# Performance work log

Measured on AMD Instinct MI355X. Metric: run time of the kernel, lower is better.

The kernel has to match this reference:

```python
import jax, jax.numpy as jnp
import numpy as np

N, E = 10000, 160000
IN_C, HID, K = 128, 256, 16


def setup_inputs() -> dict:
    key = jax.random.key(0)
    ks = jax.random.split(key, 8)
    x = jax.random.normal(ks[0], (N, IN_C), jnp.float32)
    edge_index = jax.random.randint(ks[1], (2, E), 0, N, dtype=jnp.int32).astype(jnp.int64)
    edge_attributes = jax.random.uniform(ks[2], (E,), jnp.float32)
    W1 = jax.random.normal(ks[3], (IN_C, HID), jnp.float32) / np.sqrt(IN_C)
    b1 = jnp.zeros((HID,), jnp.float32)
    W2 = jax.random.normal(ks[4], (HID, HID), jnp.float32) / np.sqrt(HID)
    b2 = jnp.zeros((HID,), jnp.float32)
    Wp = jax.random.normal(ks[5], (HID, K), jnp.float32) / np.sqrt(HID)
    bp = jnp.zeros((K,), jnp.float32)
    return dict(x=x, edge_index=edge_index, edge_attributes=edge_attributes,
                W1=W1, b1=b1, W2=W2, b2=b2, Wp=Wp, bp=bp)


def _gcn_conv(x, src, dst, ew, W, b):
    """GCNConv with add_self_loops=True, normalize=True, edge weights."""
    n = x.shape[0]
    loop = jnp.arange(n)
    s = jnp.concatenate([src, loop])
    d = jnp.concatenate([dst, loop])
    w = jnp.concatenate([ew, jnp.ones((n,), x.dtype)])
    deg = jax.ops.segment_sum(w, d, num_segments=n)           # weighted in-degree
    dis = jnp.where(deg > 0, jax.lax.rsqrt(deg), 0.0)         # D^{-1/2}, inf -> 0
    norm = dis[s] * w * dis[d]                                # per-edge coefficient
    h = x @ W                                                 # transform first
    msg = norm[:, None] * h[s]                                # gather from source
    out = jax.ops.segment_sum(msg, d, num_segments=n)         # scatter-add to target
    return out + b


def reference(x, edge_index, edge_attributes, W1, b1, W2, b2, Wp, bp):
    src, dst = edge_index[0], edge_index[1]
    ew = edge_attributes
    h = jax.nn.relu(_gcn_conv(x, src, dst, ew, W1, b1))
    h = jax.nn.relu(_gcn_conv(h, src, dst, ew, W2, b2))

    # to_dense_adj (duplicate edges accumulate)
    adj = jnp.zeros((N, N), h.dtype).at[src, dst].add(ew)

    # DMoNPooling (dropout=0, eval): s = softmax(Linear(h))
    s = jax.nn.softmax(h @ Wp + bp, axis=-1)                  # [N, K]

    out_adj = s.T @ adj @ s                                   # [K, K]
    deg = adj.sum(axis=1)                                     # [N]
    m = deg.sum() / 2
    ca = s.T @ deg[:, None]                                   # [K, 1]
    cb = deg[None, :] @ s                                     # [1, K]
    normalizer = (ca @ cb) / (2 * m)
    spectral_loss = -jnp.trace(out_adj - normalizer) / (2 * m)

    cluster_size = s.sum(axis=0)                              # [K]
    cluster_loss = jnp.linalg.norm(cluster_size) / N * jnp.sqrt(jnp.float32(K)) - 1.0

    loss = 100.0 * (spectral_loss + cluster_loss)
    # PyG returns s with a leading batch dim of 1
    return s[None], loss, 100.0 * spectral_loss, 100.0 * cluster_loss
```

## Files before the change

### kernel.cpp

```cpp
#include <hip/hip_runtime.h>
#include <math.h>


#define ER_BLOCKS 512

typedef unsigned short u16;
typedef __attribute__((ext_vector_type(8))) short short8v;
typedef __attribute__((ext_vector_type(4))) float float4v;
typedef __attribute__((ext_vector_type(4))) unsigned short ushort4v;
typedef __attribute__((ext_vector_type(8))) unsigned short ushort8v;

__device__ __forceinline__ u16 f2bf_rne(float x) {
  unsigned u = __float_as_uint(x);
  u = (u + 0x7fffu + ((u >> 16) & 1u)) >> 16;
  return (u16)u;
}
__device__ __forceinline__ float bf2f(u16 h) {
  return __uint_as_float(((unsigned)h) << 16);
}

__device__ __forceinline__ bool ei_is_i64(const int* __restrict__ ei) {
  return ((ei[1] | ei[3] | ei[5] | ei[7]) == 0);
}
__device__ __forceinline__ int ld_idx(const int* __restrict__ ei, int pos, bool i64) {
  return i64 ? ei[2 * pos] : ei[pos];
}

__global__ __launch_bounds__(256) void setup_kernel(int4* __restrict__ zp, int zn4,
                                                    const float* __restrict__ x,
                                                    u16* __restrict__ xbf, int nx4,
                                                    const float* __restrict__ W1,
                                                    u16* __restrict__ w1hi, u16* __restrict__ w1lo,
                                                    const float* __restrict__ W2,
                                                    u16* __restrict__ w2hi, u16* __restrict__ w2lo) {
  const int T1 = 256 * 128, T2 = 256 * 256;
  int idx = blockIdx.x * 256 + threadIdx.x;
  if (idx < zn4) {
    zp[idx] = make_int4(0, 0, 0, 0);
    return;
  }
  idx -= zn4;
  if (idx < nx4) {
    float4 v = reinterpret_cast<const float4*>(x)[idx];
    ushort4v o = {f2bf_rne(v.x), f2bf_rne(v.y), f2bf_rne(v.z), f2bf_rne(v.w)};
    reinterpret_cast<ushort4v*>(xbf)[idx] = o;
    return;
  }
  idx -= nx4;
  if (idx < T1) {
    int n = idx >> 7, k = idx & 127;
    float v = W1[k * 256 + n];
    u16 h = f2bf_rne(v);
    w1hi[idx] = h;
    w1lo[idx] = f2bf_rne(v - bf2f(h));
    return;
  }
  idx -= T1;
  if (idx < T2) {
    int n = idx >> 8, k = idx & 255;
    float v = W2[k * 256 + n];
    u16 h = f2bf_rne(v);
    w2hi[idx] = h;
    w2lo[idx] = f2bf_rne(v - bf2f(h));
  }
}

__global__ __launch_bounds__(256) void edge_count(const int* __restrict__ ei,
                                                  const float* __restrict__ ew,
                                                  int* __restrict__ cnt,
                                                  float* __restrict__ deg,
                                                  float* __restrict__ wdeg, int E) {
  int e = blockIdx.x * 256 + threadIdx.x;
  if (e >= E) return;
  bool i64 = ei_is_i64(ei);
  int s = ld_idx(ei, e, i64);
  int d = ld_idx(ei, E + e, i64);
  float we = ew[e];
  atomicAdd(&cnt[d], 1);
  atomicAdd(&deg[d], we);
  atomicAdd(&wdeg[s], we);
}

__global__ __launch_bounds__(1024) void scan_kernel(const int* __restrict__ cnt,
                                                    int* __restrict__ rowptr, int n) {
  __shared__ int sums[1024];
  int tid = threadIdx.x;
  int CH = (n + 1023) >> 10;
  int beg = tid * CH, end = min(beg + CH, n);
  int s = 0;
  for (int i = beg; i < end; ++i) s += cnt[i];
  sums[tid] = s;
  __syncthreads();
  for (int off = 1; off < 1024; off <<= 1) {
    int v = (tid >= off) ? sums[tid - off] : 0;
    __syncthreads();
    sums[tid] += v;
    __syncthreads();
  }
  int run = (tid == 0) ? 0 : sums[tid - 1];
  for (int i = beg; i < end; ++i) { rowptr[i] = run; run += cnt[i]; }
  if (tid == 1023) rowptr[n] = run;
}

__global__ __launch_bounds__(256) void scatter_edges(const int* __restrict__ ei,
                                                     const float* __restrict__ ew,
                                                     const int* __restrict__ rowptr,
                                                     int* __restrict__ cur,
                                                     const float* __restrict__ deg,
                                                     int* __restrict__ col,
                                                     float* __restrict__ coef, int E) {
  int e = blockIdx.x * 256 + threadIdx.x;
  if (e >= E) return;
  bool i64 = ei_is_i64(ei);
  int s = ld_idx(ei, e, i64);
  int d = ld_idx(ei, E + e, i64);
  int p = rowptr[d] + atomicAdd(&cur[d], 1);
  col[p] = s;
  float ds = 1.0f / sqrtf(deg[s] + 1.0f);
  float dd = 1.0f / sqrtf(deg[d] + 1.0f);
  coef[p] = ds * ew[e] * dd;
}

template <int CH>
__global__ __launch_bounds__(256) void aggregate_pre(const u16* __restrict__ src,
                                                     const int* __restrict__ rowptr,
                                                     const int* __restrict__ col,
                                                     const float* __restrict__ coef,
                                                     const float* __restrict__ deg,
                                                     u16* __restrict__ ohi,
                                                     u16* __restrict__ olo, int N) {
  constexpr int Q = CH / 8;
  constexpr int NS = 256 / Q;
  int i = blockIdx.x;
  int t = threadIdx.x;
  int q = t % Q, slot = t / Q;
  int e0 = rowptr[i], e1 = rowptr[i + 1];
  float a[8] = {};
  for (int p = e0 + slot; p < e1; p += NS) {
    int c = col[p];
    float w = coef[p];
    ushort8v v = *reinterpret_cast<const ushort8v*>(&src[(size_t)c * CH + q * 8]);
#pragma unroll
    for (int j = 0; j < 8; ++j) a[j] += w * bf2f(v[j]);
  }
  __shared__ float red[256][9];
#pragma unroll
  for (int j = 0; j < 8; ++j) red[t][j] = a[j];
  __syncthreads();
  if (slot == 0) {
#pragma unroll
    for (int s2 = 1; s2 < NS; ++s2)
#pragma unroll
      for (int j = 0; j < 8; ++j) a[j] += red[s2 * Q + q][j];
    float w0 = 1.0f / (deg[i] + 1.0f);
    ushort8v xv = *reinterpret_cast<const ushort8v*>(&src[(size_t)i * CH + q * 8]);
    ushort8v hv, lv;
#pragma unroll
    for (int j = 0; j < 8; ++j) {
      a[j] += w0 * bf2f(xv[j]);
      u16 h = f2bf_rne(a[j]);
      hv[j] = h;
      lv[j] = f2bf_rne(a[j] - bf2f(h));
    }
    *reinterpret_cast<ushort8v*>(&ohi[(size_t)i * CH + q * 8]) = hv;
    *reinterpret_cast<ushort8v*>(&olo[(size_t)i * CH + q * 8]) = lv;
  }
}

__global__ __launch_bounds__(256) void gemm_mfma(const u16* __restrict__ Ahi,
                                                 const u16* __restrict__ Alo,
                                                 const u16* __restrict__ Wthi,
                                                 const u16* __restrict__ Wtlo,
                                                 const float* __restrict__ bias,
                                                 float* __restrict__ C,
                                                 u16* __restrict__ Cbf,
                                                 int M, int K, int outbf) {
  __shared__ u16 As_hi[64][40], As_lo[64][40];
  __shared__ u16 Bs_hi[64][40], Bs_lo[64][40];
  int tid = threadIdx.x;
  int w = tid >> 6, l = tid & 63;
  int wm = w >> 1, wn = w & 1;
  int row0 = blockIdx.x * 64, col0 = blockIdx.y * 64;
  int srow = tid >> 2, sc = (tid & 3) * 8;
  int fr = l & 15, kg = (l >> 4) * 8;

  float4v acc[2][2];
#pragma unroll
  for (int i = 0; i < 2; ++i)
#pragma unroll
    for (int j = 0; j < 2; ++j) acc[i][j] = (float4v){0.f, 0.f, 0.f, 0.f};

  for (int k0 = 0; k0 < K; k0 += 32) {
    {
      int gr = row0 + srow;
      uint4 zero = make_uint4(0, 0, 0, 0);
      uint4 vh = zero, vl = zero;
      if (gr < M) {
        vh = *reinterpret_cast<const uint4*>(&Ahi[(size_t)gr * K + k0 + sc]);
        vl = *reinterpret_cast<const uint4*>(&Alo[(size_t)gr * K + k0 + sc]);
      }
      *reinterpret_cast<uint4*>(&As_hi[srow][sc]) = vh;
      *reinterpret_cast<uint4*>(&As_lo[srow][sc]) = vl;
      int bn = col0 + srow;
      uint4 bh = *reinterpret_cast<const uint4*>(&Wthi[(size_t)bn * K + k0 + sc]);
      uint4 bl = *reinterpret_cast<const uint4*>(&Wtlo[(size_t)bn * K + k0 + sc]);
      *reinterpret_cast<uint4*>(&Bs_hi[srow][sc]) = bh;
      *reinterpret_cast<uint4*>(&Bs_lo[srow][sc]) = bl;
    }
    __syncthreads();
    short8v ah[2], al[2], bh[2], bl[2];
#pragma unroll
    for (int i = 0; i < 2; ++i) {
      int r = wm * 32 + i * 16 + fr;
      ah[i] = *reinterpret_cast<const short8v*>(&As_hi[r][kg]);
      al[i] = *reinterpret_cast<const short8v*>(&As_lo[r][kg]);
    }
#pragma unroll
    for (int j = 0; j < 2; ++j) {
      int n = wn * 32 + j * 16 + fr;
      bh[j] = *reinterpret_cast<const short8v*>(&Bs_hi[n][kg]);
      bl[j] = *reinterpret_cast<const short8v*>(&Bs_lo[n][kg]);
    }
#pragma unroll
    for (int i = 0; i < 2; ++i)
#pragma unroll
      for (int j = 0; j < 2; ++j) {
        acc[i][j] = __builtin_amdgcn_mfma_f32_16x16x32_bf16(ah[i], bh[j], acc[i][j], 0, 0, 0);
        acc[i][j] = __builtin_amdgcn_mfma_f32_16x16x32_bf16(al[i], bh[j], acc[i][j], 0, 0, 0);
        acc[i][j] = __builtin_amdgcn_mfma_f32_16x16x32_bf16(ah[i], bl[j], acc[i][j], 0, 0, 0);
      }
    __syncthreads();
  }
#pragma unroll
  for (int j = 0; j < 2; ++j) {
    int gc = col0 + wn * 32 + j * 16 + fr;
    float bj = bias[gc];
#pragma unroll
    for (int i = 0; i < 2; ++i) {
#pragma unroll
      for (int r = 0; r < 4; ++r) {
        int gr = row0 + wm * 32 + i * 16 + (l >> 4) * 4 + r;
        if (gr < M) {
          float v = fmaxf(acc[i][j][r] + bj, 0.0f);
          if (outbf) Cbf[(size_t)gr * 256 + gc] = f2bf_rne(v);
          else       C[(size_t)gr * 256 + gc] = v;
        }
      }
    }
  }
}

__global__ __launch_bounds__(256) void pool_kernel(const float* __restrict__ h,
                                                   const float* __restrict__ Wp,
                                                   const float* __restrict__ bp,
                                                   const float* __restrict__ wdeg,
                                                   float* __restrict__ s_out,
                                                   float* __restrict__ pp, int N) {
  __shared__ float Wps[256 * 16];
  __shared__ float loc[33];
  int tid = threadIdx.x;
  for (int idx = tid; idx < 4096; idx += 256) Wps[idx] = Wp[idx];
  if (tid < 33) loc[tid] = 0.f;
  __syncthreads();
  int lane = tid & 63;
  int wave = tid >> 6;
  int k = lane & 15, g = lane >> 4;
  int node = blockIdx.x * 16 + wave * 4 + g;
  float acc = 0.f, wd = 0.f;
  if (node < N) {
    wd = wdeg[node];
    const float4* hrow = reinterpret_cast<const float4*>(h + (size_t)node * 256);
#pragma unroll 8
    for (int c4 = 0; c4 < 64; ++c4) {
      float4 hv = hrow[c4];
      int cb = c4 * 4;
      acc += hv.x * Wps[(cb + 0) * 16 + k];
      acc += hv.y * Wps[(cb + 1) * 16 + k];
      acc += hv.z * Wps[(cb + 2) * 16 + k];
      acc += hv.w * Wps[(cb + 3) * 16 + k];
    }
    acc += bp[k];
  }
  float mx = acc;
#pragma unroll
  for (int off = 1; off < 16; off <<= 1) mx = fmaxf(mx, __shfl_xor(mx, off));
  float ex = (node < N) ? expf(acc - mx) : 0.f;
  float sm = ex;
#pragma unroll
  for (int off = 1; off < 16; off <<= 1) sm += __shfl_xor(sm, off);
  float sval = (node < N) ? ex / sm : 0.f;
  if (node < N) s_out[(size_t)node * 16 + k] = sval;
  float v = sval;
  float v2 = wd * sval;
  float v3 = (k == 0) ? wd : 0.f;
  v += __shfl_xor(v, 16);  v += __shfl_xor(v, 32);
  v2 += __shfl_xor(v2, 16); v2 += __shfl_xor(v2, 32);
  v3 += __shfl_xor(v3, 16); v3 += __shfl_xor(v3, 32);
  if (lane < 16) {
    atomicAdd(&loc[lane], v);
    atomicAdd(&loc[16 + lane], v2);
  }
  if (lane == 0) atomicAdd(&loc[32], v3);
  __syncthreads();
  if (tid < 33) pp[(size_t)blockIdx.x * 33 + tid] = loc[tid];
}

__global__ __launch_bounds__(256) void edge_reduce(const int* __restrict__ ei,
                                                   const float* __restrict__ ew,
                                                   const float* __restrict__ s,
                                                   float* __restrict__ part, int E) {
  int tid = threadIdx.x;
  bool i64 = ei_is_i64(ei);
  int le = tid >> 2, sub = tid & 3;
  int epi = gridDim.x * 64;
  float acc = 0.f;
  for (int e = blockIdx.x * 64 + le; e < E; e += epi) {
    int a = ld_idx(ei, e, i64);
    int b = ld_idx(ei, E + e, i64);
    float w = ew[e];
    float4 av = *reinterpret_cast<const float4*>(s + (size_t)a * 16 + sub * 4);
    float4 bv = *reinterpret_cast<const float4*>(s + (size_t)b * 16 + sub * 4);
    float d = av.x * bv.x + av.y * bv.y + av.z * bv.z + av.w * bv.w;
    d += __shfl_xor(d, 1);
    d += __shfl_xor(d, 2);
    acc += w * d;
  }
#pragma unroll
  for (int off = 4; off < 64; off <<= 1) acc += __shfl_xor(acc, off);
  __shared__ float loc;
  if (tid == 0) loc = 0.f;
  __syncthreads();
  if ((tid & 63) == 0) atomicAdd(&loc, acc);
  __syncthreads();
  if (tid == 0) part[blockIdx.x] = loc;
}

__global__ __launch_bounds__(256) void finalize(const float* __restrict__ epart,
                                                const float* __restrict__ pp, int pb,
                                                float* __restrict__ out,
                                                int N, int s_elems) {
  __shared__ float cred[256];
  __shared__ float vals[32];
  __shared__ float scal[2];
  int tid = threadIdx.x;
  float a = 0.f;
  for (int b = tid; b < ER_BLOCKS; b += 256) a += epart[b];
  float wv = 0.f;
  for (int b = tid; b < pb; b += 256) wv += pp[(size_t)b * 33 + 32];
#pragma unroll
  for (int off = 1; off < 64; off <<= 1) {
    a += __shfl_xor(a, off);
    wv += __shfl_xor(wv, off);
  }
  if (tid == 0) { scal[0] = 0.f; scal[1] = 0.f; }
  __syncthreads();
  if ((tid & 63) == 0) {
    atomicAdd(&scal[0], a);
    atomicAdd(&scal[1], wv);
  }
  {
    int k = tid & 31, sl = tid >> 5;
    float c = 0.f;
    for (int b = sl; b < pb; b += 8) c += pp[(size_t)b * 33 + k];
    cred[tid] = c;
  }
  __syncthreads();
  if (tid < 32) {
    float c = cred[tid];
#pragma unroll
    for (int sl = 1; sl < 8; ++sl) c += cred[sl * 32 + tid];
    vals[tid] = c;
  }
  __syncthreads();
  if (tid == 0) {
    float tr = scal[0], m2 = scal[1];
    float ca2 = 0.f, cs2 = 0.f;
    for (int k = 0; k < 16; ++k) {
      cs2 += vals[k] * vals[k];
      ca2 += vals[16 + k] * vals[16 + k];
    }
    float sp = -(tr - ca2 / m2) / m2;
    float cl = sqrtf(cs2) / (float)N * 4.0f - 1.0f;
    out[s_elems + 0] = 100.f * (sp + cl);
    out[s_elems + 1] = 100.f * sp;
    out[s_elems + 2] = 100.f * cl;
  }
}

extern "C" void kernel_launch(void* const* d_in, const int* in_sizes, int n_in,
                              void* d_out, int out_size, void* d_ws, size_t ws_size,
                              hipStream_t stream) {
  const float* x  = (const float*)d_in[0];
  const int*   ei = (const int*)d_in[1];
  const float* ew = (const float*)d_in[2];
  const float* W1 = (const float*)d_in[3];
  const float* b1 = (const float*)d_in[4];
  const float* W2 = (const float*)d_in[5];
  const float* b2 = (const float*)d_in[6];
  const float* Wp = (const float*)d_in[7];
  const float* bp = (const float*)d_in[8];
  float* out = (float*)d_out;

  const int IN_C = 128, HID = 256;
  const int N = in_sizes[0] / IN_C;
  const int E = in_sizes[2];
  const int pool_blocks = (N + 15) / 16;

  char* p = (char*)d_ws;
  auto alloc = [&](size_t b) { char* r = p; p += (b + 255) & ~(size_t)255; return r; };
  float* deg     = (float*)alloc((size_t)N * 4);
  float* wdeg    = (float*)alloc((size_t)N * 4);
  int*   cnt     = (int*)alloc((size_t)N * 4);
  int*   cur     = (int*)alloc((size_t)N * 4);
  char*  zero_end = p;
  u16*   xbf     = (u16*)alloc((size_t)N * IN_C * 2);
  u16*   hbf     = (u16*)alloc((size_t)N * HID * 2);
  u16*   axhi    = (u16*)alloc((size_t)N * IN_C * 2);
  u16*   axlo    = (u16*)alloc((size_t)N * IN_C * 2);
  u16*   ahhi    = (u16*)alloc((size_t)N * HID * 2);
  u16*   ahlo    = (u16*)alloc((size_t)N * HID * 2);
  float* h2      = (float*)alloc((size_t)N * HID * 4);
  u16*   w1hi    = (u16*)alloc((size_t)256 * 128 * 2);
  u16*   w1lo    = (u16*)alloc((size_t)256 * 128 * 2);
  u16*   w2hi    = (u16*)alloc((size_t)256 * 256 * 2);
  u16*   w2lo    = (u16*)alloc((size_t)256 * 256 * 2);
  int*   rowptr  = (int*)alloc((size_t)(N + 1) * 4);
  int*   col     = (int*)alloc((size_t)E * 4);
  float* coef    = (float*)alloc((size_t)E * 4);
  float* epart   = (float*)alloc((size_t)ER_BLOCKS * 4);
  float* pp      = (float*)alloc((size_t)pool_blocks * 33 * 4);
  if ((size_t)(p - (char*)d_ws) > ws_size) return;

  int zn4 = (int)((zero_end - (char*)deg) >> 4);
  int nx4 = (N * IN_C) / 4;
  int setup_items = zn4 + nx4 + 256 * 128 + 256 * 256;
  setup_kernel<<<(setup_items + 255) / 256, 256, 0, stream>>>(
      (int4*)deg, zn4, x, xbf, nx4, W1, w1hi, w1lo, W2, w2hi, w2lo);

  int eb = (E + 255) / 256;
  edge_count<<<eb, 256, 0, stream>>>(ei, ew, cnt, deg, wdeg, E);
  scan_kernel<<<1, 1024, 0, stream>>>(cnt, rowptr, N);
  scatter_edges<<<eb, 256, 0, stream>>>(ei, ew, rowptr, cur, deg, col, coef, E);

  dim3 gg((N + 63) / 64, HID / 64);
  aggregate_pre<128><<<N, 256, 0, stream>>>(xbf, rowptr, col, coef, deg, axhi, axlo, N);
  gemm_mfma<<<gg, 256, 0, stream>>>(axhi, axlo, w1hi, w1lo, b1, nullptr, hbf, N, IN_C, 1);
  aggregate_pre<256><<<N, 256, 0, stream>>>(hbf, rowptr, col, coef, deg, ahhi, ahlo, N);
  gemm_mfma<<<gg, 256, 0, stream>>>(ahhi, ahlo, w2hi, w2lo, b2, h2, nullptr, N, HID, 0);

  pool_kernel<<<pool_blocks, 256, 0, stream>>>(h2, Wp, bp, wdeg, out, pp, N);
  edge_reduce<<<ER_BLOCKS, 256, 0, stream>>>(ei, ew, out, epart, E);
  finalize<<<1, 256, 0, stream>>>(epart, pp, pool_blocks, out, N, N * 16);
}
```

Before: 144.4 us.

## Fuse setup kernels, use wave-per-node aggregation, last-block finalize

Several independent changes. Edge counting is merged with the bf16 conversion kernel and records a per-edge rank, so scatter no longer needs a second atomic counter. The degree rsqrt is computed once per node inside the scan kernel. Aggregation now assigns one wavefront per node and reduces with shuffles instead of a 256-thread block with shared-memory reduction. The finalize kernel is folded into edge_reduce via a last-block atomic counter. These aim to cut launch count, atomics, shared-memory syncs and idle threads on low-degree nodes, at the cost of an extra rank buffer and a threadfence-based completion pattern.

Measured after the change: 178.8 us. 1.24x slower.

```diff
diff --git a/kernel.cpp b/kernel.cpp
--- a/kernel.cpp
+++ b/kernel.cpp
@@ -26,20 +26,39 @@
   return i64 ? ei[2 * pos] : ei[pos];
 }
 
-__global__ __launch_bounds__(256) void setup_kernel(int4* __restrict__ zp, int zn4,
-                                                    const float* __restrict__ x,
-                                                    u16* __restrict__ xbf, int nx4,
-                                                    const float* __restrict__ W1,
-                                                    u16* __restrict__ w1hi, u16* __restrict__ w1lo,
-                                                    const float* __restrict__ W2,
-                                                    u16* __restrict__ w2hi, u16* __restrict__ w2lo) {
+__global__ __launch_bounds__(256) void zero_init(int4* __restrict__ p, int n4) {
+  int i = blockIdx.x * 256 + threadIdx.x;
+  if (i < n4) p[i] = make_int4(0, 0, 0, 0);
+}
+
+__global__ __launch_bounds__(256) void count_convert(const int* __restrict__ ei,
+                                                     const float* __restrict__ ew,
+                                                     int* __restrict__ cnt,
+                                                     float* __restrict__ deg,
+                                                     float* __restrict__ wdeg,
+                                                     int* __restrict__ rank, int E,
+                                                     const float* __restrict__ x,
+                                                     u16* __restrict__ xbf, int nx4,
+                                                     const float* __restrict__ W1,
+                                                     u16* __restrict__ w1hi, u16* __restrict__ w1lo,
+                                                     const float* __restrict__ W2,
+                                                     u16* __restrict__ w2hi, u16* __restrict__ w2lo) {
   const int T1 = 256 * 128, T2 = 256 * 256;
-  int idx = blockIdx.x * 256 + threadIdx.x;
-  if (idx < zn4) {
-    zp[idx] = make_int4(0, 0, 0, 0);
+  int eb = (E + 255) >> 8;
+  int b = blockIdx.x;
+  if (b < eb) {
+    int e = b * 256 + threadIdx.x;
+    if (e >= E) return;
+    bool i64 = ei_is_i64(ei);
+    int s = ld_idx(ei, e, i64);
+    int d = ld_idx(ei, E + e, i64);
+    float we = ew[e];
+    rank[e] = atomicAdd(&cnt[d], 1);
+    atomicAdd(&deg[d], we);
+    atomicAdd(&wdeg[s], we);
     return;
   }
-  idx -= zn4;
+  int idx = (b - eb) * 256 + threadIdx.x;
   if (idx < nx4) {
     float4 v = reinterpret_cast<const float4*>(x)[idx];
     ushort4v o = {f2bf_rne(v.x), f2bf_rne(v.y), f2bf_rne(v.z), f2bf_rne(v.w)};
@@ -65,26 +84,13 @@
   }
 }
 
-__global__ __launch_bounds__(256) void edge_count(const int* __restrict__ ei,
-                                                  const float* __restrict__ ew,
-                                                  int* __restrict__ cnt,
-                                                  float* __restrict__ deg,
-                                                  float* __restrict__ wdeg, int E) {
-  int e = blockIdx.x * 256 + threadIdx.x;
-  if (e >= E) return;
-  bool i64 = ei_is_i64(ei);
-  int s = ld_idx(ei, e, i64);
-  int d = ld_idx(ei, E + e, i64);
-  float we = ew[e];
-  atomicAdd(&cnt[d], 1);
-  atomicAdd(&deg[d], we);
-  atomicAdd(&wdeg[s], we);
-}
-
-__global__ __launch_bounds__(1024) void scan_kernel(const int* __restrict__ cnt,
-                                                    int* __restrict__ rowptr, int n) {
+__global__ __launch_bounds__(1024) void scan_dis(const int* __restrict__ cnt,
+                                                 int* __restrict__ rowptr,
+                                                 const float* __restrict__ deg,
+                                                 float* __restrict__ dis, int n) {
   __shared__ int sums[1024];
   int tid = threadIdx.x;
+  for (int i = tid; i < n; i += 1024) dis[i] = 1.0f / sqrtf(deg[i] + 1.0f);
   int CH = (n + 1023) >> 10;
   int beg = tid * CH, end = min(beg + CH, n);
   int s = 0;
@@ -105,8 +111,8 @@
 __global__ __launch_bounds__(256) void scatter_edges(const int* __restrict__ ei,
                                                      const float* __restrict__ ew,
                                                      const int* __restrict__ rowptr,
-                                                     int* __restrict__ cur,
-                                                     const float* __restrict__ deg,
+                                                     const int* __restrict__ rank,
+                                                     const float* __restrict__ dis,
                                                      int* __restrict__ col,
                                                      float* __restrict__ coef, int E) {
   int e = blockIdx.x * 256 + threadIdx.x;
@@ -114,11 +120,9 @@
   bool i64 = ei_is_i64(ei);
   int s = ld_idx(ei, e, i64);
   int d = ld_idx(ei, E + e, i64);
-  int p = rowptr[d] + atomicAdd(&cur[d], 1);
+  int p = rowptr[d] + rank[e];
   col[p] = s;
-  float ds = 1.0f / sqrtf(deg[s] + 1.0f);
-  float dd = 1.0f / sqrtf(deg[d] + 1.0f);
-  coef[p] = ds * ew[e] * dd;
+  coef[p] = dis[s] * ew[e] * dis[d];
 }
 
 template <int CH>
@@ -130,10 +134,12 @@
                                                      u16* __restrict__ ohi,
                                                      u16* __restrict__ olo, int N) {
   constexpr int Q = CH / 8;
-  constexpr int NS = 256 / Q;
-  int i = blockIdx.x;
-  int t = threadIdx.x;
-  int q = t % Q, slot = t / Q;
+  constexpr int NS = 64 / Q;
+  int wave = threadIdx.x >> 6;
+  int lane = threadIdx.x & 63;
+  int i = blockIdx.x * 4 + wave;
+  if (i >= N) return;
+  int q = lane % Q, slot = lane / Q;
   int e0 = rowptr[i], e1 = rowptr[i + 1];
   float a[8] = {};
   for (int p = e0 + slot; p < e1; p += NS) {
@@ -143,15 +149,13 @@
 #pragma unroll
     for (int j = 0; j < 8; ++j) a[j] += w * bf2f(v[j]);
   }
-  __shared__ float red[256][9];
-#pragma unroll
-  for (int j = 0; j < 8; ++j) red[t][j] = a[j];
-  __syncthreads();
+  if constexpr (NS == 4) {
+#pragma unroll
+    for (int j = 0; j < 8; ++j) a[j] += __shfl_xor(a[j], 16);
+  }
+#pragma unroll
+  for (int j = 0; j < 8; ++j) a[j] += __shfl_xor(a[j], 32);
   if (slot == 0) {
-#pragma unroll
-    for (int s2 = 1; s2 < NS; ++s2)
-#pragma unroll
-      for (int j = 0; j < 8; ++j) a[j] += red[s2 * Q + q][j];
     float w0 = 1.0f / (deg[i] + 1.0f);
     ushort8v xv = *reinterpret_cast<const ushort8v*>(&src[(size_t)i * CH + q * 8]);
     ushort8v hv, lv;
@@ -308,7 +312,11 @@
 __global__ __launch_bounds__(256) void edge_reduce(const int* __restrict__ ei,
                                                    const float* __restrict__ ew,
                                                    const float* __restrict__ s,
-                                                   float* __restrict__ part, int E) {
+                                                   float* __restrict__ part,
+                                                   const float* __restrict__ pp, int pb,
+                                                   int* __restrict__ ctr,
+                                                   float* __restrict__ out,
+                                                   int N, int s_elems, int E) {
   int tid = threadIdx.x;
   bool i64 = ei_is_i64(ei);
   int le = tid >> 2, sub = tid & 3;
@@ -333,18 +341,18 @@
   if ((tid & 63) == 0) atomicAdd(&loc, acc);
   __syncthreads();
   if (tid == 0) part[blockIdx.x] = loc;
-}
-
-__global__ __launch_bounds__(256) void finalize(const float* __restrict__ epart,
-                                                const float* __restrict__ pp, int pb,
-                                                float* __restrict__ out,
-                                                int N, int s_elems) {
+
+  __shared__ bool amLast;
+  __threadfence();
+  if (tid == 0) amLast = (atomicAdd(ctr, 1) == (int)gridDim.x - 1);
+  __syncthreads();
+  if (!amLast) return;
+
   __shared__ float cred[256];
   __shared__ float vals[32];
   __shared__ float scal[2];
-  int tid = threadIdx.x;
   float a = 0.f;
-  for (int b = tid; b < ER_BLOCKS; b += 256) a += epart[b];
+  for (int b = tid; b < (int)gridDim.x; b += 256) a += part[b];
   float wv = 0.f;
   for (int b = tid; b < pb; b += 256) wv += pp[(size_t)b * 33 + 32];
 #pragma unroll
@@ -411,7 +419,7 @@
   float* deg     = (float*)alloc((size_t)N * 4);
   float* wdeg    = (float*)alloc((size_t)N * 4);
   int*   cnt     = (int*)alloc((size_t)N * 4);
-  int*   cur     = (int*)alloc((size_t)N * 4);
+  int*   ctr     = (int*)alloc(256);
   char*  zero_end = p;
   u16*   xbf     = (u16*)alloc((size_t)N * IN_C * 2);
   u16*   hbf     = (u16*)alloc((size_t)N * HID * 2);
@@ -420,11 +428,13 @@
   u16*   ahhi    = (u16*)alloc((size_t)N * HID * 2);
   u16*   ahlo    = (u16*)alloc((size_t)N * HID * 2);
   float* h2      = (float*)alloc((size_t)N * HID * 4);
+  float* dis     = (float*)alloc((size_t)N * 4);
   u16*   w1hi    = (u16*)alloc((size_t)256 * 128 * 2);
   u16*   w1lo    = (u16*)alloc((size_t)256 * 128 * 2);
   u16*   w2hi    = (u16*)alloc((size_t)256 * 256 * 2);
   u16*   w2lo    = (u16*)alloc((size_t)256 * 256 * 2);
   int*   rowptr  = (int*)alloc((size_t)(N + 1) * 4);
+  int*   rank    = (int*)alloc((size_t)E * 4);
   int*   col     = (int*)alloc((size_t)E * 4);
   float* coef    = (float*)alloc((size_t)E * 4);
   float* epart   = (float*)alloc((size_t)ER_BLOCKS * 4);
@@ -432,23 +442,25 @@
   if ((size_t)(p - (char*)d_ws) > ws_size) return;
 
   int zn4 = (int)((zero_end - (char*)deg) >> 4);
+  zero_init<<<(zn4 + 255) / 256, 256, 0, stream>>>((int4*)deg, zn4);
+
+  int eb = (E + 255) / 256;
   int nx4 = (N * IN_C) / 4;
-  int setup_items = zn4 + nx4 + 256 * 128 + 256 * 256;
-  setup_kernel<<<(setup_items + 255) / 256, 256, 0, stream>>>(
-      (int4*)deg, zn4, x, xbf, nx4, W1, w1hi, w1lo, W2, w2hi, w2lo);
-
-  int eb = (E + 255) / 256;
-  edge_count<<<eb, 256, 0, stream>>>(ei, ew, cnt, deg, wdeg, E);
-  scan_kernel<<<1, 1024, 0, stream>>>(cnt, rowptr, N);
-  scatter_edges<<<eb, 256, 0, stream>>>(ei, ew, rowptr, cur, deg, col, coef, E);
+  int conv_items = nx4 + 256 * 128 + 256 * 256;
+  int cc_blocks = eb + (conv_items + 255) / 256;
+  count_convert<<<cc_blocks, 256, 0, stream>>>(ei, ew, cnt, deg, wdeg, rank, E,
+                                               x, xbf, nx4, W1, w1hi, w1lo,
+                                               W2, w2hi, w2lo);
+  scan_dis<<<1, 1024, 0, stream>>>(cnt, rowptr, deg, dis, N);
+  scatter_edges<<<eb, 256, 0, stream>>>(ei, ew, rowptr, rank, dis, col, coef, E);
 
   dim3 gg((N + 63) / 64, HID / 64);
-  aggregate_pre<128><<<N, 256, 0, stream>>>(xbf, rowptr, col, coef, deg, axhi, axlo, N);
+  aggregate_pre<128><<<(N + 3) / 4, 256, 0, stream>>>(xbf, rowptr, col, coef, deg, axhi, axlo, N);
   gemm_mfma<<<gg, 256, 0, stream>>>(axhi, axlo, w1hi, w1lo, b1, nullptr, hbf, N, IN_C, 1);
-  aggregate_pre<256><<<N, 256, 0, stream>>>(hbf, rowptr, col, coef, deg, ahhi, ahlo, N);
+  aggregate_pre<256><<<(N + 3) / 4, 256, 0, stream>>>(hbf, rowptr, col, coef, deg, ahhi, ahlo, N);
   gemm_mfma<<<gg, 256, 0, stream>>>(ahhi, ahlo, w2hi, w2lo, b2, h2, nullptr, N, HID, 0);
 
   pool_kernel<<<pool_blocks, 256, 0, stream>>>(h2, Wp, bp, wdeg, out, pp, N);
-  edge_reduce<<<ER_BLOCKS, 256, 0, stream>>>(ei, ew, out, epart, E);
-  finalize<<<1, 256, 0, stream>>>(epart, pp, pool_blocks, out, N, N * 16);
-}
+  edge_reduce<<<ER_BLOCKS, 256, 0, stream>>>(ei, ew, out, epart, pp, pool_blocks,
+                                             ctr, out, N, N * 16, E);
+}
```
